# Performance work log

Hardware: AMD Instinct MI355X
Metric: run time of the kernel (lower is better)

Reference implementation:

```python
import jax, jax.numpy as jnp
import numpy as np

INPUT_SIZE = 32      # activity vocab
HIDDEN = 128
OUTPUT = 33          # 32 act logits + 1 duration
NUM_LAYERS = 2
MAX_LEN = 256
SOS = 0


def setup_inputs() -> dict:
    key = jax.random.key(0)
    ks = jax.random.split(key, 16)
    s = 0.05
    inp = {
        "batch_size": 8192,
        "hidden": jax.random.normal(ks[0], (NUM_LAYERS, 8192, HIDDEN), jnp.float32),
        # CustomEmbedding: embed act index to hidden-1 dims, concat raw duration -> hidden dims
        "emb": jax.random.normal(ks[1], (INPUT_SIZE, HIDDEN - 1), jnp.float32) * s,
        # torch.nn.GRU params, gate order (r, z, n)
        "w_ih_0": jax.random.normal(ks[2], (3 * HIDDEN, HIDDEN), jnp.float32) * s,
        "w_hh_0": jax.random.normal(ks[3], (3 * HIDDEN, HIDDEN), jnp.float32) * s,
        "b_ih_0": jax.random.normal(ks[4], (3 * HIDDEN,), jnp.float32) * s,
        "b_hh_0": jax.random.normal(ks[5], (3 * HIDDEN,), jnp.float32) * s,
        "w_ih_1": jax.random.normal(ks[6], (3 * HIDDEN, HIDDEN), jnp.float32) * s,
        "w_hh_1": jax.random.normal(ks[7], (3 * HIDDEN, HIDDEN), jnp.float32) * s,
        "b_ih_1": jax.random.normal(ks[8], (3 * HIDDEN,), jnp.float32) * s,
        "b_hh_1": jax.random.normal(ks[9], (3 * HIDDEN,), jnp.float32) * s,
        "fc_w": jax.random.normal(ks[10], (OUTPUT, HIDDEN), jnp.float32) * s,
        "fc_b": jax.random.normal(ks[11], (OUTPUT,), jnp.float32) * s,
    }
    return inp


def _gru_cell(x, h, w_ih, w_hh, b_ih, b_hh):
    gi = x @ w_ih.T + b_ih          # [B, 3H]
    gh = h @ w_hh.T + b_hh
    ir, iz, inn = jnp.split(gi, 3, axis=-1)
    hr, hz, hn = jnp.split(gh, 3, axis=-1)
    r = jax.nn.sigmoid(ir + hr)
    z = jax.nn.sigmoid(iz + hz)
    n = jnp.tanh(inn + r * hn)
    return (1.0 - z) * n + z * h


def _decode(batch_size, hidden, emb, w_ih_0, w_hh_0, b_ih_0, b_hh_0,
            w_ih_1, w_hh_1, b_ih_1, b_hh_1, fc_w, fc_b):
    B = batch_size
    # decoder_input [B, 2]: (act_index_as_float, duration); sos index = 0
    init_inp = jnp.zeros((B, 2), hidden.dtype).at[:, 0].set(float(SOS))

    def step(carry, _):
        inp, h = carry
        act = inp[:, 0].astype(jnp.int32)
        x = jnp.concatenate([emb[act], inp[:, 1:2]], axis=-1)   # [B, H]
        h0 = _gru_cell(x, h[0], w_ih_0, w_hh_0, b_ih_0, b_hh_0)
        h1 = _gru_cell(h0, h[1], w_ih_1, w_hh_1, b_ih_1, b_hh_1)
        pred = h1 @ fc_w.T + fc_b                                # [B, O]
        # pack(): argmax over act logits; softmax over a size-1 seq dim == 1.0
        topi = jnp.argmax(pred[:, : OUTPUT - 1], axis=-1)
        nxt = jnp.concatenate(
            [topi.astype(pred.dtype)[:, None], jnp.ones((B, 1), pred.dtype)], axis=-1)
        return (nxt, jnp.stack([h0, h1])), pred

    _, outs = jax.lax.scan(step, (init_inp, hidden), None, length=MAX_LEN)
    outs = jnp.transpose(outs, (1, 0, 2))                        # [B, T, O]
    acts_logits = outs[..., : OUTPUT - 1]
    durations = jax.nn.softmax(outs[..., OUTPUT - 1:], axis=1)   # softmax over time
    log_probs = jnp.concatenate(
        [jax.nn.log_softmax(acts_logits, axis=-1), durations], axis=-1)
    probs = jnp.concatenate(
        [jax.nn.softmax(acts_logits, axis=-1), durations], axis=-1)
    return log_probs, probs


def reference(batch_size, hidden, emb, w_ih_0, w_hh_0, b_ih_0, b_hh_0,
              w_ih_1, w_hh_1, b_ih_1, b_hh_1, fc_w, fc_b):
    return _decode(batch_size, hidden, emb, w_ih_0, w_hh_0, b_ih_0, b_hh_0,
                   w_ih_1, w_hh_1, b_ih_1, b_hh_1, fc_w, fc_b)
```

## Files before the change

kernel.cpp:

```cpp
#include <hip/hip_runtime.h>

#define HDIM  128
#define G3    384
#define RPB   32
#define NTHR  512
#define NSTEP 256
#define NOUT  33
#define BROWS 8192
#define NBLK  (BROWS / RPB)
#define LOGP_ELEMS 69206016LL
#define PRED_LD 34

typedef _Float16 half8 __attribute__((ext_vector_type(8)));
typedef float    f32x4 __attribute__((ext_vector_type(4)));

#define HS0_OFF   0
#define HS1_OFF   16384
#define BST_OFF   32768
#define PRED_OFF  131072
#define ACTS_OFF  135424
#define LDS_BYTES 135552

#define WP_BYTES  294912
#define FP_BYTES  24576

__device__ __forceinline__ float sigf(float x) { return 1.0f / (1.0f + __expf(-x)); }
__device__ __forceinline__ float tanh_fast(float x) { return 1.0f - 2.0f / (__expf(2.0f*x) + 1.0f); }

__global__ void prep_kernel(const float* __restrict__ emb, const float* __restrict__ wih0,
                            const float* __restrict__ bih0, float* __restrict__ T1,
                            float* __restrict__ T0) {
    int a = blockIdx.x;
    int g = threadIdx.x;
    const float* e = emb + a * 127;
    const float* w = wih0 + g * HDIM;
    float s = bih0[g];
    for (int k = 0; k < 127; ++k) s += e[k] * w[k];
    T1[a * G3 + g] = s + w[127];
    if (a == 0) T0[g] = s;
}

__global__ void prep_pack(const float* __restrict__ whh0, const float* __restrict__ wih1,
                          const float* __restrict__ whh1, const float* __restrict__ fcw,
                          half8* __restrict__ WP) {
    int b = blockIdx.x;
    int tid  = threadIdx.x;
    int lane = tid & 63;
    int kc   = tid >> 6;
    bool isfc = (b >= 72);
    if (!isfc) {
        int mat = b / 24, nt = b % 24;
        const float* W = (mat == 0) ? whh0 : (mat == 1) ? wih1 : whh1;
        int g = nt * 16 + (lane & 15);
        int k = kc * 32 + (lane >> 4) * 8;
        half8 v1;
#pragma unroll
        for (int e = 0; e < 8; ++e) v1[e] = (_Float16)W[g * HDIM + k + e];
        WP[(size_t)(((mat * 24 + nt) * 4 + kc)) * 64 + lane] = v1;
    } else {
        int nt = b - 72;
        int g = nt * 16 + (lane & 15);
        int k = kc * 32 + (lane >> 4) * 8;
        half8 v1, v2;
#pragma unroll
        for (int e = 0; e < 8; ++e) {
            float x = (g >= NOUT) ? 0.0f : fcw[g * HDIM + k + e];
            _Float16 s1 = (_Float16)x;
            v1[e] = s1; v2[e] = (_Float16)(x - (float)s1);
        }
        size_t base = (size_t)(WP_BYTES / 1024 + (nt * 4 + kc) * 2) * 64 + lane;
        WP[base]      = v1;
        WP[base + 64] = v2;
    }
}

__launch_bounds__(NTHR, 2)
__global__ void decoder_kernel(const float* __restrict__ hid,
                               const float* __restrict__ T1, const float* __restrict__ T0,
                               const char* __restrict__ Bpg,
                               const float* __restrict__ bhh0,
                               const float* __restrict__ bih1, const float* __restrict__ bhh1,
                               const float* __restrict__ fcb,
                               float* __restrict__ out) {
    extern __shared__ char smraw[];
    char*  hs0   = smraw + HS0_OFF;
    char*  hs1   = smraw + HS1_OFF;
    char*  bst   = smraw + BST_OFF;
    float* preds = (float*)(smraw + PRED_OFF);
    int*   acts  = (int*)(smraw + ACTS_OFF);

    const int tid  = threadIdx.x;
    const int row0 = blockIdx.x * RPB;
    float* lp = out;
    float* pp = out + LOGP_ELEMS;

    const int lane  = tid & 63;
    const int w     = tid >> 6;
    const int col   = lane & 15;
    const int q     = lane >> 4;
    const int akoff = q * 16;
    const int j     = w * 16 + col;
    char* const mybuf = bst + (size_t)w * 12288;

    const float bG0 = bhh0[j],       bG1 = bhh0[128 + j], bG2 = bhh0[256 + j];
    const float bH0 = bhh1[j],       bH1 = bhh1[128 + j], bH2 = bhh1[256 + j];
    const float bI0 = bih1[j],       bI1 = bih1[128 + j], bI2 = bih1[256 + j];

    const int fnt = w % 3, fMt = (w / 3) & 1;
    const int fo  = fnt * 16 + col;
    const float fbias = (fo < NOUT) ? fcb[fo] : 0.0f;
    half8 fcr[4][2];
#pragma unroll
    for (int kc = 0; kc < 4; ++kc)
#pragma unroll
        for (int s = 0; s < 2; ++s)
            fcr[kc][s] = *(const half8*)(Bpg + WP_BYTES +
                (size_t)(((fnt * 4 + kc) * 2 + s) * 1024) + lane * 16);

    float h0v[2][4], h1v[2][4];
#pragma unroll
    for (int Mt = 0; Mt < 2; ++Mt)
#pragma unroll
        for (int i = 0; i < 4; ++i) {
            int row = Mt * 16 + q * 4 + i;
            float v0 = hid[(size_t)(row0 + row) * HDIM + j];
            float v1 = hid[(size_t)BROWS * HDIM + (size_t)(row0 + row) * HDIM + j];
            h0v[Mt][i] = v0; h1v[Mt][i] = v1;
            int off = (row * 256 + j * 2) ^ ((row & 7) << 4);
            _Float16 s1 = (_Float16)v0, s2 = (_Float16)(v0 - (float)s1);
            *(_Float16*)(hs0 + off) = s1;
            *(_Float16*)(hs0 + 8192 + off) = s2;
            s1 = (_Float16)v1; s2 = (_Float16)(v1 - (float)s1);
            *(_Float16*)(hs1 + off) = s1;
            *(_Float16*)(hs1 + 8192 + off) = s2;
        }
    asm volatile("s_waitcnt lgkmcnt(0)" ::: "memory");
    __builtin_amdgcn_s_barrier();

#define LGKM0() asm volatile("s_waitcnt lgkmcnt(0)" ::: "memory")
#define VMW()   asm volatile("s_waitcnt vmcnt(9)" ::: "memory")
#define BAR()   __builtin_amdgcn_s_barrier()
#define MFMA(a, b, c) __builtin_amdgcn_mfma_f32_16x16x32_f16((a), (b), (c), 0, 0, 0)

#define STAGE3(G_) do {                                                           \
        int gm_  = (G_) % 12;                                                     \
        int mat_ = (gm_ < 4) ? 0 : ((gm_ < 8) ? 2 : 1);                           \
        int kc_  = gm_ & 3;                                                       \
        char* db_ = mybuf + (size_t)(3 * ((G_) & 3)) * 1024;                      \
        _Pragma("unroll")                                                         \
        for (int ty_ = 0; ty_ < 3; ++ty_) {                                       \
            const char* src_ = Bpg + (size_t)(((mat_ * 24 + (ty_ * 8 + w)) * 4 + kc_) * 1024) + lane * 16; \
            __builtin_amdgcn_global_load_lds((const unsigned int*)src_,           \
                                             (unsigned int*)(db_ + ty_ * 1024), 16, 0, 0); \
        }                                                                         \
    } while (0)

#define GROUP(G_, HS_, ACC_) do {                                                 \
        STAGE3((G_) + 3);                                                         \
        VMW();                                                                    \
        int kc_ = (G_) & 3;                                                       \
        half8 a1_[2], a2_[2];                                                     \
        _Pragma("unroll")                                                         \
        for (int Mt_ = 0; Mt_ < 2; ++Mt_) {                                       \
            int row_ = Mt_ * 16 + col;                                            \
            int off_ = (row_ * 256 + kc_ * 64 + akoff) ^ ((row_ & 7) << 4);       \
            a1_[Mt_] = *(const half8*)((HS_) + off_);                             \
            a2_[Mt_] = *(const half8*)((HS_) + 8192 + off_);                      \
        }                                                                         \
        char* db_ = mybuf + (size_t)(3 * ((G_) & 3)) * 1024;                      \
        half8 b0_ = *(const half8*)(db_ + lane * 16);                             \
        half8 b1_ = *(const half8*)(db_ + 1024 + lane * 16);                      \
        half8 b2_ = *(const half8*)(db_ + 2048 + lane * 16);                      \
        _Pragma("unroll")                                                         \
        for (int Mt_ = 0; Mt_ < 2; ++Mt_) {                                       \
            ACC_[0][Mt_] = MFMA(a1_[Mt_], b0_, ACC_[0][Mt_]);                     \
            ACC_[0][Mt_] = MFMA(a2_[Mt_], b0_, ACC_[0][Mt_]);                     \
        }                                                                         \
        _Pragma("unroll")                                                         \
        for (int Mt_ = 0; Mt_ < 2; ++Mt_) {                                       \
            ACC_[1][Mt_] = MFMA(a1_[Mt_], b1_, ACC_[1][Mt_]);                     \
            ACC_[1][Mt_] = MFMA(a2_[Mt_], b1_, ACC_[1][Mt_]);                     \
        }                                                                         \
        _Pragma("unroll")                                                         \
        for (int Mt_ = 0; Mt_ < 2; ++Mt_) {                                       \
            ACC_[2][Mt_] = MFMA(a1_[Mt_], b2_, ACC_[2][Mt_]);                     \
            ACC_[2][Mt_] = MFMA(a2_[Mt_], b2_, ACC_[2][Mt_]);                     \
        }                                                                         \
    } while (0)

    STAGE3(0); STAGE3(1); STAGE3(2);

#pragma unroll 1
    for (int t = 0; t < NSTEP; ++t) {
        float gi[3][2][4];
        if (t == 0) {
            float g0v = T0[j], g1v = T0[128 + j], g2v = T0[256 + j];
#pragma unroll
            for (int Mt = 0; Mt < 2; ++Mt)
#pragma unroll
                for (int i = 0; i < 4; ++i) {
                    gi[0][Mt][i] = g0v; gi[1][Mt][i] = g1v; gi[2][Mt][i] = g2v;
                }
        } else {
#pragma unroll
            for (int Mt = 0; Mt < 2; ++Mt)
#pragma unroll
                for (int i = 0; i < 4; ++i) {
                    const float* tab = T1 + acts[Mt * 16 + q * 4 + i] * G3;
                    gi[0][Mt][i] = tab[j];
                    gi[1][Mt][i] = tab[128 + j];
                    gi[2][Mt][i] = tab[256 + j];
                }
        }

        f32x4 g0[3][2], ah[3][2];
        {
            f32x4 v0 = {bG0, bG0, bG0, bG0}, v1 = {bG1, bG1, bG1, bG1}, v2 = {bG2, bG2, bG2, bG2};
            g0[0][0] = v0; g0[0][1] = v0; g0[1][0] = v1; g0[1][1] = v1; g0[2][0] = v2; g0[2][1] = v2;
            f32x4 u0 = {bH0, bH0, bH0, bH0}, u1 = {bH1, bH1, bH1, bH1}, u2 = {bH2, bH2, bH2, bH2};
            ah[0][0] = u0; ah[0][1] = u0; ah[1][0] = u1; ah[1][1] = u1; ah[2][0] = u2; ah[2][1] = u2;
        }
        GROUP(0, hs0, g0); GROUP(1, hs0, g0); GROUP(2, hs0, g0); GROUP(3, hs0, g0);
        GROUP(4, hs1, ah); GROUP(5, hs1, ah); GROUP(6, hs1, ah); GROUP(7, hs1, ah);
        LGKM0(); BAR();

#pragma unroll
        for (int Mt = 0; Mt < 2; ++Mt)
#pragma unroll
            for (int i = 0; i < 4; ++i) {
                float rg = sigf(gi[0][Mt][i] + g0[0][Mt][i]);
                float zg = sigf(gi[1][Mt][i] + g0[1][Mt][i]);
                float ng = tanh_fast(gi[2][Mt][i] + rg * g0[2][Mt][i]);
                float hnew = (1.0f - zg) * ng + zg * h0v[Mt][i];
                h0v[Mt][i] = hnew;
                int row = Mt * 16 + q * 4 + i;
                int off = (row * 256 + j * 2) ^ ((row & 7) << 4);
                _Float16 s1 = (_Float16)hnew, s2 = (_Float16)(hnew - (float)s1);
                *(_Float16*)(hs0 + off) = s1;
                *(_Float16*)(hs0 + 8192 + off) = s2;
            }
        LGKM0(); BAR();

        f32x4 ai[3][2];
        {
            f32x4 v0 = {bI0, bI0, bI0, bI0}, v1 = {bI1, bI1, bI1, bI1}, v2 = {bI2, bI2, bI2, bI2};
            ai[0][0] = v0; ai[0][1] = v0; ai[1][0] = v1; ai[1][1] = v1; ai[2][0] = v2; ai[2][1] = v2;
        }
        GROUP(8, hs0, ai); GROUP(9, hs0, ai); GROUP(10, hs0, ai); GROUP(11, hs0, ai);

#pragma unroll
        for (int Mt = 0; Mt < 2; ++Mt)
#pragma unroll
            for (int i = 0; i < 4; ++i) {
                float rg = sigf(ai[0][Mt][i] + ah[0][Mt][i]);
                float zg = sigf(ai[1][Mt][i] + ah[1][Mt][i]);
                float ng = tanh_fast(ai[2][Mt][i] + rg * ah[2][Mt][i]);
                float hnew = (1.0f - zg) * ng + zg * h1v[Mt][i];
                h1v[Mt][i] = hnew;
                int row = Mt * 16 + q * 4 + i;
                int off = (row * 256 + j * 2) ^ ((row & 7) << 4);
                _Float16 s1 = (_Float16)hnew, s2 = (_Float16)(hnew - (float)s1);
                *(_Float16*)(hs1 + off) = s1;
                *(_Float16*)(hs1 + 8192 + off) = s2;
            }
        LGKM0(); BAR();

        if (w < 6) {
            f32x4 acc = {fbias, fbias, fbias, fbias};
#pragma unroll
            for (int kc = 0; kc < 4; ++kc) {
                int row = fMt * 16 + col;
                int off = (row * 256 + kc * 64 + akoff) ^ ((row & 7) << 4);
                half8 a1 = *(const half8*)(hs1 + off);
                half8 a2 = *(const half8*)(hs1 + 8192 + off);
                acc = MFMA(a1, fcr[kc][0], acc);
                acc = MFMA(a2, fcr[kc][0], acc);
                acc = MFMA(a1, fcr[kc][1], acc);
            }
            if (fo < NOUT) {
#pragma unroll
                for (int i = 0; i < 4; ++i)
                    preds[(fMt * 16 + q * 4 + i) * PRED_LD + fo] = acc[i];
            }
        }
        LGKM0(); BAR();

        {
            int r = tid >> 4; int l16 = tid & 15; int c0 = l16 * 2;
            float v0 = preds[r * PRED_LD + c0];
            float v1 = preds[r * PRED_LD + c0 + 1];
            float bv; int bi;
            if (v0 >= v1) { bv = v0; bi = c0; } else { bv = v1; bi = c0 + 1; }
#pragma unroll
            for (int d = 1; d < 16; d <<= 1) {
                float ov = __shfl_xor(bv, d);
                int   oi = __shfl_xor(bi, d);
                if (ov > bv || (ov == bv && oi < bi)) { bv = ov; bi = oi; }
            }
            float e0 = __expf(v0 - bv), e1 = __expf(v1 - bv);
            float s = e0 + e1;
#pragma unroll
            for (int d = 1; d < 16; d <<= 1) s += __shfl_xor(s, d);
            float ls = __logf(s);
            float inv = 1.0f / s;
            size_t base = ((size_t)(row0 + r) * NSTEP + t) * NOUT;
            lp[base + c0]     = v0 - bv - ls;
            lp[base + c0 + 1] = v1 - bv - ls;
            pp[base + c0]     = e0 * inv;
            pp[base + c0 + 1] = e1 * inv;
            if (l16 == 0) {
                acts[r] = bi;
                lp[base + 32] = preds[r * PRED_LD + 32];
            }
        }
        LGKM0(); BAR();
    }
#undef STAGE3
#undef GROUP
#undef LGKM0
#undef VMW
#undef BAR
#undef MFMA
}

__global__ void dur_kernel(float* __restrict__ out) {
    int wid  = threadIdx.x >> 6;
    int lane = threadIdx.x & 63;
    int row  = blockIdx.x * 4 + wid;
    float* lp = out;
    float* pp = out + LOGP_ELEMS;
    size_t base = (size_t)row * NSTEP * NOUT + 32;

    float v[4]; float m = -1e30f;
#pragma unroll
    for (int i = 0; i < 4; ++i) {
        v[i] = lp[base + (size_t)(lane * 4 + i) * NOUT];
        m = fmaxf(m, v[i]);
    }
#pragma unroll
    for (int d = 1; d < 64; d <<= 1) m = fmaxf(m, __shfl_xor(m, d));
    float e[4]; float s = 0.0f;
#pragma unroll
    for (int i = 0; i < 4; ++i) { e[i] = __expf(v[i] - m); s += e[i]; }
#pragma unroll
    for (int d = 1; d < 64; d <<= 1) s += __shfl_xor(s, d);
    float inv = 1.0f / s;
#pragma unroll
    for (int i = 0; i < 4; ++i) {
        size_t idx = base + (size_t)(lane * 4 + i) * NOUT;
        float dv = e[i] * inv;
        lp[idx] = dv;
        pp[idx] = dv;
    }
}

extern "C" void kernel_launch(void* const* d_in, const int* in_sizes, int n_in,
                              void* d_out, int out_size, void* d_ws, size_t ws_size,
                              hipStream_t stream) {
    const float* hid  = (const float*)d_in[1];
    const float* emb  = (const float*)d_in[2];
    const float* wih0 = (const float*)d_in[3];
    const float* whh0 = (const float*)d_in[4];
    const float* bih0 = (const float*)d_in[5];
    const float* bhh0 = (const float*)d_in[6];
    const float* wih1 = (const float*)d_in[7];
    const float* whh1 = (const float*)d_in[8];
    const float* bih1 = (const float*)d_in[9];
    const float* bhh1 = (const float*)d_in[10];
    const float* fcw  = (const float*)d_in[11];
    const float* fcb  = (const float*)d_in[12];

    char*  ws = (char*)d_ws;
    half8* WP = (half8*)ws;
    float* T1 = (float*)(ws + WP_BYTES + FP_BYTES);
    float* T0 = T1 + 32 * G3;

    prep_kernel<<<32, 384, 0, stream>>>(emb, wih0, bih0, T1, T0);
    prep_pack<<<75, 256, 0, stream>>>(whh0, wih1, whh1, fcw, WP);

    hipFuncSetAttribute((const void*)decoder_kernel,
                        hipFuncAttributeMaxDynamicSharedMemorySize, LDS_BYTES);
    decoder_kernel<<<NBLK, NTHR, LDS_BYTES, stream>>>(
        hid, T1, T0, ws, bhh0, bih1, bhh1, fcb, (float*)d_out);

    dur_kernel<<<BROWS / 4, 256, 0, stream>>>((float*)d_out);
}
```

Before: 3.040 ms.

## Fuse FC and argmax into every wave redundantly, removing two barriers per step

Every wave now computes the FC projection for all 32 rows, with transposed MFMA operands read from an LDS copy of the FC weights. Argmax is done in registers with cross-lane shuffles, and the chosen action is taken from the wave's own result. This removes the preds/acts LDS round trip and two block barriers per timestep. The FC/softmax for step t runs at the start of step t+1, and layer‑0's hidden update is interleaved with the remaining layer‑1 recurrent MFMA groups. The cost is 8x redundant FC MFMA work per block and about 20 KB more LDS, which may lower occupancy.

```diff
diff --git a/kernel.cpp b/kernel.cpp
--- a/kernel.cpp
+++ b/kernel.cpp
@@ -9,7 +9,6 @@
 #define BROWS 8192
 #define NBLK  (BROWS / RPB)
 #define LOGP_ELEMS 69206016LL
-#define PRED_LD 34
 
 typedef _Float16 half8 __attribute__((ext_vector_type(8)));
 typedef float    f32x4 __attribute__((ext_vector_type(4)));
@@ -17,9 +16,8 @@
 #define HS0_OFF   0
 #define HS1_OFF   16384
 #define BST_OFF   32768
-#define PRED_OFF  131072
-#define ACTS_OFF  135424
-#define LDS_BYTES 135552
+#define FCL_OFF   131072
+#define LDS_BYTES 155648
 
 #define WP_BYTES  294912
 #define FP_BYTES  24576
@@ -83,11 +81,10 @@
                                const float* __restrict__ fcb,
                                float* __restrict__ out) {
     extern __shared__ char smraw[];
-    char*  hs0   = smraw + HS0_OFF;
-    char*  hs1   = smraw + HS1_OFF;
-    char*  bst   = smraw + BST_OFF;
-    float* preds = (float*)(smraw + PRED_OFF);
-    int*   acts  = (int*)(smraw + ACTS_OFF);
+    char*  hs0 = smraw + HS0_OFF;
+    char*  hs1 = smraw + HS1_OFF;
+    char*  bst = smraw + BST_OFF;
+    char*  fcl = smraw + FCL_OFF;
 
     const int tid  = threadIdx.x;
     const int row0 = blockIdx.x * RPB;
@@ -106,16 +103,20 @@
     const float bH0 = bhh1[j],       bH1 = bhh1[128 + j], bH2 = bhh1[256 + j];
     const float bI0 = bih1[j],       bI1 = bih1[128 + j], bI2 = bih1[256 + j];
 
-    const int fnt = w % 3, fMt = (w / 3) & 1;
-    const int fo  = fnt * 16 + col;
-    const float fbias = (fo < NOUT) ? fcb[fo] : 0.0f;
-    half8 fcr[4][2];
-#pragma unroll
-    for (int kc = 0; kc < 4; ++kc)
-#pragma unroll
-        for (int s = 0; s < 2; ++s)
-            fcr[kc][s] = *(const half8*)(Bpg + WP_BYTES +
-                (size_t)(((fnt * 4 + kc) * 2 + s) * 1024) + lane * 16);
+    f32x4 fcbr[3];
+#pragma unroll
+    for (int t2 = 0; t2 < 3; ++t2)
+#pragma unroll
+        for (int i = 0; i < 4; ++i) {
+            int o = 16 * t2 + q * 4 + i;
+            fcbr[t2][i] = (o < NOUT) ? fcb[o] : 0.0f;
+        }
+
+    {
+        const uint4* src = (const uint4*)(Bpg + WP_BYTES);
+        uint4* dst = (uint4*)fcl;
+        for (int i = tid; i < FP_BYTES / 16; i += NTHR) dst[i] = src[i];
+    }
 
     float h0v[2][4], h1v[2][4];
 #pragma unroll
@@ -134,8 +135,7 @@
             *(_Float16*)(hs1 + off) = s1;
             *(_Float16*)(hs1 + 8192 + off) = s2;
         }
-    asm volatile("s_waitcnt lgkmcnt(0)" ::: "memory");
-    __builtin_amdgcn_s_barrier();
+    __syncthreads();
 
 #define LGKM0() asm volatile("s_waitcnt lgkmcnt(0)" ::: "memory")
 #define VMW()   asm volatile("s_waitcnt vmcnt(9)" ::: "memory")
@@ -188,6 +188,80 @@
         }                                                                         \
     } while (0)
 
+#define FC_SOFTMAX(TOUT_, ACTS_) do {                                             \
+        f32x4 facc[2][3];                                                         \
+        _Pragma("unroll")                                                         \
+        for (int Mt_ = 0; Mt_ < 2; ++Mt_)                                         \
+            _Pragma("unroll")                                                     \
+            for (int t2_ = 0; t2_ < 3; ++t2_) facc[Mt_][t2_] = fcbr[t2_];         \
+        _Pragma("unroll")                                                         \
+        for (int kc_ = 0; kc_ < 4; ++kc_) {                                       \
+            half8 a1_[2], a2_[2];                                                 \
+            _Pragma("unroll")                                                     \
+            for (int Mt_ = 0; Mt_ < 2; ++Mt_) {                                   \
+                int row_ = Mt_ * 16 + col;                                        \
+                int off_ = (row_ * 256 + kc_ * 64 + akoff) ^ ((row_ & 7) << 4);   \
+                a1_[Mt_] = *(const half8*)(hs1 + off_);                           \
+                a2_[Mt_] = *(const half8*)(hs1 + 8192 + off_);                    \
+            }                                                                     \
+            _Pragma("unroll")                                                     \
+            for (int t2_ = 0; t2_ < 3; ++t2_) {                                   \
+                half8 f1_ = *(const half8*)(fcl + ((t2_ * 4 + kc_) * 2 + 0) * 1024 + lane * 16); \
+                half8 f2_ = *(const half8*)(fcl + ((t2_ * 4 + kc_) * 2 + 1) * 1024 + lane * 16); \
+                _Pragma("unroll")                                                 \
+                for (int Mt_ = 0; Mt_ < 2; ++Mt_) {                               \
+                    facc[Mt_][t2_] = MFMA(f1_, a1_[Mt_], facc[Mt_][t2_]);         \
+                    facc[Mt_][t2_] = MFMA(f1_, a2_[Mt_], facc[Mt_][t2_]);         \
+                    facc[Mt_][t2_] = MFMA(f2_, a1_[Mt_], facc[Mt_][t2_]);         \
+                }                                                                 \
+            }                                                                     \
+        }                                                                         \
+        _Pragma("unroll")                                                         \
+        for (int Mt_ = 0; Mt_ < 2; ++Mt_) {                                       \
+            float bv_ = facc[Mt_][0][0]; int bi_ = q * 4;                         \
+            _Pragma("unroll")                                                     \
+            for (int t2_ = 0; t2_ < 2; ++t2_)                                     \
+                _Pragma("unroll")                                                 \
+                for (int i_ = 0; i_ < 4; ++i_) {                                  \
+                    if (t2_ == 0 && i_ == 0) continue;                            \
+                    float v_ = facc[Mt_][t2_][i_];                                \
+                    int   o_ = 16 * t2_ + q * 4 + i_;                             \
+                    if (v_ > bv_) { bv_ = v_; bi_ = o_; }                         \
+                }                                                                 \
+            _Pragma("unroll")                                                     \
+            for (int d_ = 16; d_ <= 32; d_ <<= 1) {                               \
+                float ov_ = __shfl_xor(bv_, d_);                                  \
+                int   oi_ = __shfl_xor(bi_, d_);                                  \
+                if (ov_ > bv_ || (ov_ == bv_ && oi_ < bi_)) { bv_ = ov_; bi_ = oi_; } \
+            }                                                                     \
+            (ACTS_)[Mt_] = bi_;                                                   \
+            if (w == Mt_) {                                                       \
+                float ex_[2][4]; float s_ = 0.0f;                                 \
+                _Pragma("unroll")                                                 \
+                for (int t2_ = 0; t2_ < 2; ++t2_)                                 \
+                    _Pragma("unroll")                                             \
+                    for (int i_ = 0; i_ < 4; ++i_) {                              \
+                        ex_[t2_][i_] = __expf(facc[Mt_][t2_][i_] - bv_);          \
+                        s_ += ex_[t2_][i_];                                       \
+                    }                                                             \
+                s_ += __shfl_xor(s_, 16);                                         \
+                s_ += __shfl_xor(s_, 32);                                         \
+                float ls_ = __logf(s_), inv_ = 1.0f / s_;                         \
+                int r_ = lane & 15;                                               \
+                size_t base_ = ((size_t)(row0 + Mt_ * 16 + r_) * NSTEP + (TOUT_)) * NOUT; \
+                _Pragma("unroll")                                                 \
+                for (int t2_ = 0; t2_ < 2; ++t2_)                                 \
+                    _Pragma("unroll")                                             \
+                    for (int i_ = 0; i_ < 4; ++i_) {                              \
+                        int o_ = 16 * t2_ + q * 4 + i_;                           \
+                        lp[base_ + o_] = facc[Mt_][t2_][i_] - bv_ - ls_;          \
+                        pp[base_ + o_] = ex_[t2_][i_] * inv_;                     \
+                    }                                                             \
+                if (q == 0) lp[base_ + 32] = facc[Mt_][2][0];                     \
+            }                                                                     \
+        }                                                                         \
+    } while (0)
+
     STAGE3(0); STAGE3(1); STAGE3(2);
 
 #pragma unroll 1
@@ -202,11 +276,14 @@
                     gi[0][Mt][i] = g0v; gi[1][Mt][i] = g1v; gi[2][Mt][i] = g2v;
                 }
         } else {
+            int actsR[2];
+            FC_SOFTMAX(t - 1, actsR);
 #pragma unroll
             for (int Mt = 0; Mt < 2; ++Mt)
 #pragma unroll
                 for (int i = 0; i < 4; ++i) {
-                    const float* tab = T1 + acts[Mt * 16 + q * 4 + i] * G3;
+                    int act = __shfl(actsR[Mt], q * 4 + i);
+                    const float* tab = T1 + act * G3;
                     gi[0][Mt][i] = tab[j];
                     gi[1][Mt][i] = tab[128 + j];
                     gi[2][Mt][i] = tab[256 + j];
@@ -221,9 +298,9 @@
             ah[0][0] = u0; ah[0][1] = u0; ah[1][0] = u1; ah[1][1] = u1; ah[2][0] = u2; ah[2][1] = u2;
         }
         GROUP(0, hs0, g0); GROUP(1, hs0, g0); GROUP(2, hs0, g0); GROUP(3, hs0, g0);
-        GROUP(4, hs1, ah); GROUP(5, hs1, ah); GROUP(6, hs1, ah); GROUP(7, hs1, ah);
-        LGKM0(); BAR();
-
+        GROUP(4, hs1, ah); GROUP(5, hs1, ah);
+
+        _Float16 s1r[2][4], s2r[2][4];
 #pragma unroll
         for (int Mt = 0; Mt < 2; ++Mt)
 #pragma unroll
@@ -233,11 +310,21 @@
                 float ng = tanh_fast(gi[2][Mt][i] + rg * g0[2][Mt][i]);
                 float hnew = (1.0f - zg) * ng + zg * h0v[Mt][i];
                 h0v[Mt][i] = hnew;
+                s1r[Mt][i] = (_Float16)hnew;
+                s2r[Mt][i] = (_Float16)(hnew - (float)s1r[Mt][i]);
+            }
+
+        GROUP(6, hs1, ah); GROUP(7, hs1, ah);
+        LGKM0(); BAR();
+
+#pragma unroll
+        for (int Mt = 0; Mt < 2; ++Mt)
+#pragma unroll
+            for (int i = 0; i < 4; ++i) {
                 int row = Mt * 16 + q * 4 + i;
                 int off = (row * 256 + j * 2) ^ ((row & 7) << 4);
-                _Float16 s1 = (_Float16)hnew, s2 = (_Float16)(hnew - (float)s1);
-                *(_Float16*)(hs0 + off) = s1;
-                *(_Float16*)(hs0 + 8192 + off) = s2;
+                *(_Float16*)(hs0 + off) = s1r[Mt][i];
+                *(_Float16*)(hs0 + 8192 + off) = s2r[Mt][i];
             }
         LGKM0(); BAR();
 
@@ -264,59 +351,16 @@
                 *(_Float16*)(hs1 + 8192 + off) = s2;
             }
         LGKM0(); BAR();
-
-        if (w < 6) {
-            f32x4 acc = {fbias, fbias, fbias, fbias};
-#pragma unroll
-            for (int kc = 0; kc < 4; ++kc) {
-                int row = fMt * 16 + col;
-                int off = (row * 256 + kc * 64 + akoff) ^ ((row & 7) << 4);
-                half8 a1 = *(const half8*)(hs1 + off);
-                half8 a2 = *(const half8*)(hs1 + 8192 + off);
-                acc = MFMA(a1, fcr[kc][0], acc);
-                acc = MFMA(a2, fcr[kc][0], acc);
-                acc = MFMA(a1, fcr[kc][1], acc);
-            }
-            if (fo < NOUT) {
-#pragma unroll
-                for (int i = 0; i < 4; ++i)
-                    preds[(fMt * 16 + q * 4 + i) * PRED_LD + fo] = acc[i];
-            }
-        }
-        LGKM0(); BAR();
-
-        {
-            int r = tid >> 4; int l16 = tid & 15; int c0 = l16 * 2;
-            float v0 = preds[r * PRED_LD + c0];
-            float v1 = preds[r * PRED_LD + c0 + 1];
-            float bv; int bi;
-            if (v0 >= v1) { bv = v0; bi = c0; } else { bv = v1; bi = c0 + 1; }
-#pragma unroll
-            for (int d = 1; d < 16; d <<= 1) {
-                float ov = __shfl_xor(bv, d);
-                int   oi = __shfl_xor(bi, d);
-                if (ov > bv || (ov == bv && oi < bi)) { bv = ov; bi = oi; }
-            }
-            float e0 = __expf(v0 - bv), e1 = __expf(v1 - bv);
-            float s = e0 + e1;
-#pragma unroll
-            for (int d = 1; d < 16; d <<= 1) s += __shfl_xor(s, d);
-            float ls = __logf(s);
-            float inv = 1.0f / s;
-            size_t base = ((size_t)(row0 + r) * NSTEP + t) * NOUT;
-            lp[base + c0]     = v0 - bv - ls;
-            lp[base + c0 + 1] = v1 - bv - ls;
-            pp[base + c0]     = e0 * inv;
-            pp[base + c0 + 1] = e1 * inv;
-            if (l16 == 0) {
-                acts[r] = bi;
-                lp[base + 32] = preds[r * PRED_LD + 32];
-            }
-        }
-        LGKM0(); BAR();
+    }
+
+    {
+        int actsF[2];
+        FC_SOFTMAX(NSTEP - 1, actsF);
+        (void)actsF;
     }
 #undef STAGE3
 #undef GROUP
+#undef FC_SOFTMAX
 #undef LGKM0
 #undef VMW
 #undef BAR
```

After: 2.674 ms. -12.0%, faster.
